# Performance work log

Hardware: AMD Instinct MI355X
Metric: run time of the kernel (lower is better)

Reference implementation:

```python
import jax
import jax.numpy as jnp
from jax import lax
import numpy as np

B, T, IN, H, K = 8, 4096, 512, 512, 2


def setup_inputs() -> dict:
    key = jax.random.key(0)
    k = jax.random.split(key, 5)
    scale_w0 = 1.0 / np.sqrt(IN * K)
    scale_w1 = 1.0 / np.sqrt(H * K)
    return {
        "x": jax.random.normal(k[0], (B, T, IN), jnp.float32),
        "w0": jax.random.normal(k[1], (3 * H, IN, K), jnp.float32) * scale_w0,
        "b0": jax.random.normal(k[2], (3 * H,), jnp.float32) * scale_w0,
        "w1": jax.random.normal(k[3], (3 * H, H, K), jnp.float32) * scale_w1,
        "b1": jax.random.normal(k[4], (3 * H,), jnp.float32) * scale_w1,
    }


def _qrnn_layer(x, w, b):
    # x: [B, T, C]; w: [3H, C, K]; causal conv (left pad K-1), matching
    # torch padding=K-1 then slicing off the last K-1 timesteps.
    xc = jnp.transpose(x, (0, 2, 1))  # [B, C, T]
    conv = lax.conv_general_dilated(
        xc, w, window_strides=(1,), padding=[(K - 1, 0)],
        dimension_numbers=("NCH", "OIH", "NCH"))
    conv = conv + b[None, :, None]
    conv = jnp.transpose(conv, (0, 2, 1))  # [B, T, 3H]
    z, f, o = jnp.split(conv, 3, axis=-1)
    z = jnp.tanh(z)
    f = jax.nn.sigmoid(f)
    o = jax.nn.sigmoid(o)

    def step(h, zfo):
        zt, ft, ot = zfo
        h = ft * h + (1.0 - ft) * zt  # fo-pool recurrence
        return h, ot * h

    h0 = jnp.zeros((x.shape[0], z.shape[-1]), x.dtype)
    hT, outs = lax.scan(
        step, h0,
        (jnp.swapaxes(z, 0, 1), jnp.swapaxes(f, 0, 1), jnp.swapaxes(o, 0, 1)))
    return jnp.swapaxes(outs, 0, 1), hT  # [B, T, H], [B, H]


def reference(x, w0, b0, w1, b1):
    out, h0 = _qrnn_layer(x, w0, b0)
    out, h1 = _qrnn_layer(out, w1, b1)
    return out, h0, h1
```

## Files before the change

### kernel.cpp

```cpp
#include <hip/hip_runtime.h>
#include <cstdint>

#define B_ 8
#define T_ 4096
#define TP1 4097
#define IN_ 512
#define H_ 512
#define N3H 1536
#define KD 1024
#define CHUNKS 64
#define CLEN 64
#define NT 16

typedef __attribute__((ext_vector_type(4))) float floatx4;
typedef __attribute__((ext_vector_type(4))) float f4;
typedef __attribute__((ext_vector_type(8))) short short8;
typedef __attribute__((ext_vector_type(4))) unsigned short us4;
typedef __attribute__((ext_vector_type(4))) _Float16 h4;

__device__ __forceinline__ unsigned short f2bf(float v){
  unsigned int u = __float_as_uint(v);
  unsigned int r = (u + 0x7fffu + ((u >> 16) & 1u)) >> 16;
  return (unsigned short)r;
}
__device__ __forceinline__ float sigm(float x){
  return __builtin_amdgcn_rcpf(1.f + __expf(-x));
}
__device__ __forceinline__ float tanhf_(float x){ return 2.f*sigm(2.f*x) - 1.f; }

#define GLLS(src, dst) __builtin_amdgcn_global_load_lds( \
    (const __attribute__((address_space(1))) void*)(src), \
    (__attribute__((address_space(3))) void*)(dst), 16, 0, 0)

__global__ void cast_pad_kernel(const float* __restrict__ x, unsigned short* __restrict__ xpad){
  int64_t i = (int64_t)blockIdx.x*256 + threadIdx.x;
  const int64_t total = (int64_t)B_*TP1*(IN_/4);
  if (i >= total) return;
  int cg = (int)(i & 127);
  int64_t r = i >> 7;
  int t = (int)(r % TP1);
  int b = (int)(r / TP1);
  us4 o;
  if (t == 0){ o = (us4){0,0,0,0}; }
  else {
    f4 v = *(const f4*)(x + ((int64_t)b*T_ + (t-1))*IN_ + cg*4);
    #pragma unroll
    for (int u=0;u<4;++u) o[u] = f2bf(v[u]);
  }
  *(us4*)(xpad + r*IN_ + cg*4) = o;
}

__global__ void wt_kernel(const float* __restrict__ wA, unsigned short* __restrict__ wtA,
                          const float* __restrict__ wB, unsigned short* __restrict__ wtB){
  int i = blockIdx.x*256 + threadIdx.x;
  if (i >= N3H*512) return;
  const float* w = blockIdx.y ? wB : wA;
  unsigned short* wt = blockIdx.y ? wtB : wtA;
  int ci = i & 511;
  int o = i >> 9;
  const float* wp = w + (int64_t)o*KD + ci*2;
  wt[(int64_t)o*KD + ci]       = f2bf(wp[0]);
  wt[(int64_t)o*KD + 512 + ci] = f2bf(wp[1]);
}

#define MFMA(a,b,c) __builtin_amdgcn_mfma_f32_16x16x32_bf16(a,b,c,0,0,0)
#define BAR() __builtin_amdgcn_s_barrier()

#define ST_A(tt, h) do { \
    const unsigned short* _s = aSrc + (h)*128*IN_ + (tt)*64; \
    unsigned short* _d = smem + ((tt)&1)*16384 + (h)*8192 + dstBase; \
    GLLS(_s, _d); GLLS(_s + 64*IN_, _d + 4096); } while(0)
#define ST_B(tt, h) do { \
    const unsigned short* _s = bSrc + (h)*128*KD + (tt)*64; \
    unsigned short* _d = smem + 32768 + ((tt)&1)*16384 + (h)*8192 + dstBase; \
    GLLS(_s, _d); GLLS(_s + 64*KD, _d + 4096); } while(0)

#define LDA(d,h,i,s) (*(const short8*)(smem + (d)*16384 + (h)*8192 + aRd + (i)*1024 + (s)))
#define LDB(d,h,i,s) (*(const short8*)(smem + (d)*16384 + (h)*8192 + bRd + (i)*1024 + (s)))

#define TILE(tc, SA1, SB1, SA0, SB0, VMN) do { \
  const int d_ = (tc) & 1; \
   \
  _Pragma("unroll") for (int i=0;i<4;++i){ aF[i][0]=LDA(d_,0,i,sw0); aF[i][1]=LDA(d_,0,i,sw1); } \
  _Pragma("unroll") for (int j=0;j<2;++j){ bF0[j][0]=LDB(d_,0,j,sw0); bF0[j][1]=LDB(d_,0,j,sw1); } \
  if (SA1) ST_A((tc)+1, 1); \
  BAR(); \
  __builtin_amdgcn_s_setprio(1); \
  _Pragma("unroll") for (int i=0;i<4;++i) _Pragma("unroll") for (int j=0;j<2;++j){ \
    acc[i][j]=MFMA(aF[i][0],bF0[j][0],acc[i][j]); acc[i][j]=MFMA(aF[i][1],bF0[j][1],acc[i][j]); } \
  __builtin_amdgcn_s_setprio(0); \
  BAR(); \
   \
  _Pragma("unroll") for (int j=0;j<2;++j){ bF1[j][0]=LDB(d_,1,j,sw0); bF1[j][1]=LDB(d_,1,j,sw1); } \
  if (SB1) ST_B((tc)+1, 1); \
  BAR(); \
  __builtin_amdgcn_s_setprio(1); \
  _Pragma("unroll") for (int i=0;i<4;++i) _Pragma("unroll") for (int j=0;j<2;++j){ \
    acc[i][2+j]=MFMA(aF[i][0],bF1[j][0],acc[i][2+j]); acc[i][2+j]=MFMA(aF[i][1],bF1[j][1],acc[i][2+j]); } \
  __builtin_amdgcn_s_setprio(0); \
  BAR(); \
   \
  _Pragma("unroll") for (int i=0;i<4;++i){ aF[i][0]=LDA(d_,1,i,sw0); aF[i][1]=LDA(d_,1,i,sw1); } \
  if (SA0) ST_A((tc)+2, 0); \
  BAR(); \
  __builtin_amdgcn_s_setprio(1); \
  _Pragma("unroll") for (int i=0;i<4;++i) _Pragma("unroll") for (int j=0;j<2;++j){ \
    acc[4+i][j]=MFMA(aF[i][0],bF0[j][0],acc[4+i][j]); acc[4+i][j]=MFMA(aF[i][1],bF0[j][1],acc[4+i][j]); } \
  __builtin_amdgcn_s_setprio(0); \
  BAR(); \
   \
  if (SB0) ST_B((tc)+2, 0); \
  BAR(); \
  __builtin_amdgcn_s_setprio(1); \
  _Pragma("unroll") for (int i=0;i<4;++i) _Pragma("unroll") for (int j=0;j<2;++j){ \
    acc[4+i][2+j]=MFMA(aF[i][0],bF1[j][0],acc[4+i][2+j]); acc[4+i][2+j]=MFMA(aF[i][1],bF1[j][1],acc[4+i][2+j]); } \
  __builtin_amdgcn_s_setprio(0); \
  if ((VMN)==4) asm volatile("s_waitcnt vmcnt(4)" ::: "memory"); \
  else if ((VMN)==0) asm volatile("s_waitcnt vmcnt(0)" ::: "memory"); \
  BAR(); \
} while(0)

__global__ __launch_bounds__(512, 2) void gemm_kernel(
    const unsigned short* __restrict__ A, const unsigned short* __restrict__ W,
    const float* __restrict__ bias, _Float16* __restrict__ C){
  __shared__ unsigned short smem[65536];
  const int tid  = threadIdx.x;
  const int lane = tid & 63;
  const int wave = tid >> 6;
  const int l16  = lane & 15;
  const int quad = lane >> 4;
  const int wm = wave >> 2;
  const int wn = wave & 3;
  const int lrow = lane >> 3;
  const int lcol = lane & 7;

  const int bid = blockIdx.x;
  const int wg = (bid & 7) * 96 + (bid >> 3);
  const int mt = wg / 6;
  const int nt = wg % 6;
  const int m0 = mt * 256;
  const int n0 = nt * 256;
  const int bb = m0 / T_;
  const int act = n0 >> 9;

  const unsigned short* aSrc = A + (int64_t)(m0 + bb + wave*8 + lrow)*IN_ + (lcol ^ lrow)*8;
  const unsigned short* bSrc = W + (int64_t)(n0 + wave*8 + lrow)*KD + (lcol ^ lrow)*8;
  const int dstBase = (wave*8 + lrow)*64 + lcol*8;

  const int sw0 = ( quad      ^ (l16 & 7)) * 8;
  const int sw1 = ((4 ^ quad) ^ (l16 & 7)) * 8;
  const int aRd = (wm*64 + l16)*64;
  const int bRd = 32768 + (wn*32 + l16)*64;

  floatx4 acc[8][4];
  #pragma unroll
  for (int i=0;i<8;i++)
    #pragma unroll
    for (int j=0;j<4;j++) acc[i][j] = (floatx4){0.f,0.f,0.f,0.f};
  short8 aF[4][2], bF0[2][2], bF1[2][2];

  ST_A(0,0); ST_B(0,0); ST_A(0,1); ST_B(0,1); ST_A(1,0); ST_B(1,0);
  asm volatile("s_waitcnt vmcnt(4)" ::: "memory");
  BAR();

  #pragma unroll 2
  for (int t = 0; t < NT-2; ++t){
    TILE(t, 1, 1, 1, 1, 4);
  }
  TILE(NT-2, 1, 1, 0, 0, 0);
  TILE(NT-1, 0, 0, 0, 0, -1);

  float bv[4];
  #pragma unroll
  for (int n=0;n<4;++n){
    const int cb = ((n&2)?128:0) + wn*32 + (n&1)*16;
    bv[n] = bias[n0 + cb + l16];
  }
  #pragma unroll
  for (int m=0;m<8;++m){
    const int rb = ((m&4)?128:0) + wm*64 + (m&3)*16;
    const int row = m0 + rb + quad*4;
    #pragma unroll
    for (int n=0;n<4;++n){
      const int cb = ((n&2)?128:0) + wn*32 + (n&1)*16;
      const int col = n0 + cb + l16;
      _Float16* cp = C + (int64_t)row*N3H + col;
      #pragma unroll
      for (int r=0;r<4;++r){
        float v = acc[m][n][r] + bv[n];
        v = (act == 0) ? tanhf_(v) : sigm(v);
        cp[(int64_t)r*N3H] = (_Float16)v;
      }
    }
  }
}

__global__ void scan_phase1(const _Float16* __restrict__ conv,
                            float* __restrict__ carA, float* __restrict__ carB){
  int q = blockIdx.x*256 + threadIdx.x;
  int chg = q & 127;
  int bq = (q >> 7) & 7;
  int c  = q >> 10;
  int ch = chg*4;
  f4 Aa = {1.f,1.f,1.f,1.f}, Bb = {0.f,0.f,0.f,0.f};
  const _Float16* p = conv + ((int64_t)bq*T_ + c*CLEN)*N3H + ch;
  for (int g=0; g<CLEN/8; ++g){
    h4 zb[8], fb[8];
    #pragma unroll
    for (int u=0;u<8;++u){
      zb[u] = *(const h4*)(p + (int64_t)u*N3H);
      fb[u] = *(const h4*)(p + (int64_t)u*N3H + 512);
    }
    #pragma unroll
    for (int u=0;u<8;++u){
      #pragma unroll
      for (int v=0;v<4;++v){
        float fv = (float)fb[u][v];
        float zv = (float)zb[u][v];
        Aa[v] *= fv;
        Bb[v] = fv*Bb[v] + (1.f-fv)*zv;
      }
    }
    p += (int64_t)8*N3H;
  }
  *(f4*)(carA + (int64_t)q*4) = Aa;
  *(f4*)(carB + (int64_t)q*4) = Bb;
}

__global__ void scan_phase2(const float* __restrict__ carA, const float* __restrict__ carB,
                            float* __restrict__ hstart, float* __restrict__ hT){
  int q = blockIdx.x*256 + threadIdx.x;
  float h = 0.f;
  for (int c=0;c<CHUNKS;++c){
    int64_t idx = (int64_t)c*4096 + q;
    hstart[idx] = h;
    h = carA[idx]*h + carB[idx];
  }
  hT[q] = h;
}

template<int LAYER>
__global__ void scan_phase3(const _Float16* __restrict__ conv,
                            const float* __restrict__ hstart, unsigned short* __restrict__ xpad,
                            float* __restrict__ outf){
  int q = blockIdx.x*256 + threadIdx.x;
  int chg = q & 127;
  int bq = (q >> 7) & 7;
  int c  = q >> 10;
  int ch = chg*4;
  f4 h;
  #pragma unroll
  for (int v=0;v<4;++v) h[v] = hstart[(int64_t)c*4096 + bq*512 + ch + v];
  const _Float16* p = conv + ((int64_t)bq*T_ + c*CLEN)*N3H + ch;
  int t = c*CLEN;
  for (int g=0; g<CLEN/8; ++g){
    h4 zb[8], fb[8], ob[8];
    #pragma unroll
    for (int u=0;u<8;++u){
      zb[u] = *(const h4*)(p + (int64_t)u*N3H);
      fb[u] = *(const h4*)(p + (int64_t)u*N3H + 512);
      ob[u] = *(const h4*)(p + (int64_t)u*N3H + 1024);
    }
    #pragma unroll
    for (int u=0;u<8;++u){
      if (LAYER == 0){
        us4 ov4;
        #pragma unroll
        for (int v=0;v<4;++v){
          float fv = (float)fb[u][v];
          h[v] = fv*h[v] + (1.f-fv)*(float)zb[u][v];
          ov4[v] = f2bf((float)ob[u][v]*h[v]);
        }
        *(us4*)(xpad + ((int64_t)bq*TP1 + t+u + 1)*IN_ + ch) = ov4;
      } else {
        f4 of4;
        #pragma unroll
        for (int v=0;v<4;++v){
          float fv = (float)fb[u][v];
          h[v] = fv*h[v] + (1.f-fv)*(float)zb[u][v];
          of4[v] = (float)ob[u][v]*h[v];
        }
        *(f4*)(outf + ((int64_t)bq*T_ + t+u)*H_ + ch) = of4;
      }
    }
    t += 8; p += (int64_t)8*N3H;
  }
}

extern "C" void kernel_launch(void* const* d_in, const int* in_sizes, int n_in,
                              void* d_out, int out_size, void* d_ws, size_t ws_size,
                              hipStream_t stream){
  const float* x  = (const float*)d_in[0];
  const float* w0 = (const float*)d_in[1];
  const float* b0 = (const float*)d_in[2];
  const float* w1 = (const float*)d_in[3];
  const float* b1 = (const float*)d_in[4];
  float* out = (float*)d_out;

  char* ws = (char*)d_ws;
  size_t off = 0;
  auto alloc = [&](size_t bytes)->char*{
    char* p = ws + off; off = (off + bytes + 255) & ~(size_t)255; return p; };
  unsigned short* xpad = (unsigned short*)alloc((size_t)B_*TP1*IN_*2);
  unsigned short* Wt0  = (unsigned short*)alloc((size_t)N3H*KD*2);
  unsigned short* Wt1  = (unsigned short*)alloc((size_t)N3H*KD*2);
  _Float16* conv = (_Float16*)alloc((size_t)B_*T_*N3H*2);
  float* carA = (float*)alloc((size_t)CHUNKS*4096*4);
  float* carB = (float*)alloc((size_t)CHUNKS*4096*4);
  float* hst  = (float*)alloc((size_t)CHUNKS*4096*4);
  if (off > ws_size) return;

  float* out_main = out;
  float* h0 = out + (int64_t)B_*T_*H_;
  float* h1 = h0 + B_*H_;

  const int64_t padN = (int64_t)B_*TP1*(IN_/4);
  cast_pad_kernel<<<(int)((padN + 255)/256), 256, 0, stream>>>(x, xpad);
  dim3 wgrid((N3H*512 + 255)/256, 2);
  wt_kernel<<<wgrid, 256, 0, stream>>>(w0, Wt0, w1, Wt1);

  const int ggrid = ((B_*T_)/256) * (N3H/256);
  const int sgrid = (CHUNKS*8*128) / 256;
  gemm_kernel<<<ggrid, 512, 0, stream>>>(xpad, Wt0, b0, conv);
  scan_phase1<<<sgrid, 256, 0, stream>>>(conv, carA, carB);
  scan_phase2<<<16, 256, 0, stream>>>(carA, carB, hst, h0);
  scan_phase3<0><<<sgrid, 256, 0, stream>>>(conv, hst, xpad, nullptr);

  gemm_kernel<<<ggrid, 512, 0, stream>>>(xpad, Wt1, b1, conv);
  scan_phase1<<<sgrid, 256, 0, stream>>>(conv, carA, carB);
  scan_phase2<<<16, 256, 0, stream>>>(carA, carB, hst, h1);
  scan_phase3<1><<<sgrid, 256, 0, stream>>>(conv, hst, nullptr, out_main);
}
```

Baseline: 414.6 us.

## Make GEMM persistent over three N tiles, prefetching next tile across boundaries

The GEMM grid is reduced from 768 blocks to 256, and each block loops over three consecutive 256-column N tiles for one M tile. The first two K-steps of the next N tile are prefetched during the tail of the current one, so the pipeline does not drain and refill between tiles. This is meant to cut the per-block prologue and epilogue cost and the tail idle time. In exchange, the epilogue stores and activations are serialized inside the block, and only 256 blocks are available to fill the CUs.

```diff
diff --git a/kernel.cpp b/kernel.cpp
--- a/kernel.cpp
+++ b/kernel.cpp
@@ -67,23 +67,24 @@
 #define BAR() __builtin_amdgcn_s_barrier()
 
 #define ST_A(tt, h) do { \
-    const unsigned short* _s = aSrc + (h)*128*IN_ + (tt)*64; \
+    const unsigned short* _s = aSrc + (h)*128*IN_ + ((tt)&(NT-1))*64; \
     unsigned short* _d = smem + ((tt)&1)*16384 + (h)*8192 + dstBase; \
     GLLS(_s, _d); GLLS(_s + 64*IN_, _d + 4096); } while(0)
-#define ST_B(tt, h) do { \
-    const unsigned short* _s = bSrc + (h)*128*KD + (tt)*64; \
+#define ST_BX(PTR, tt, h) do { \
+    const unsigned short* _s = (PTR) + (h)*128*KD + ((tt)&(NT-1))*64; \
     unsigned short* _d = smem + 32768 + ((tt)&1)*16384 + (h)*8192 + dstBase; \
     GLLS(_s, _d); GLLS(_s + 64*KD, _d + 4096); } while(0)
+#define ST_B(tt, h) ST_BX(bSrcC, tt, h)
 
 #define LDA(d,h,i,s) (*(const short8*)(smem + (d)*16384 + (h)*8192 + aRd + (i)*1024 + (s)))
 #define LDB(d,h,i,s) (*(const short8*)(smem + (d)*16384 + (h)*8192 + bRd + (i)*1024 + (s)))
 
-#define TILE(tc, SA1, SB1, SA0, SB0, VMN) do { \
+#define TILE(tc, S0, S1, S2, S3, VMN) do { \
   const int d_ = (tc) & 1; \
    \
   _Pragma("unroll") for (int i=0;i<4;++i){ aF[i][0]=LDA(d_,0,i,sw0); aF[i][1]=LDA(d_,0,i,sw1); } \
   _Pragma("unroll") for (int j=0;j<2;++j){ bF0[j][0]=LDB(d_,0,j,sw0); bF0[j][1]=LDB(d_,0,j,sw1); } \
-  if (SA1) ST_A((tc)+1, 1); \
+  S0; \
   BAR(); \
   __builtin_amdgcn_s_setprio(1); \
   _Pragma("unroll") for (int i=0;i<4;++i) _Pragma("unroll") for (int j=0;j<2;++j){ \
@@ -92,7 +93,7 @@
   BAR(); \
    \
   _Pragma("unroll") for (int j=0;j<2;++j){ bF1[j][0]=LDB(d_,1,j,sw0); bF1[j][1]=LDB(d_,1,j,sw1); } \
-  if (SB1) ST_B((tc)+1, 1); \
+  S1; \
   BAR(); \
   __builtin_amdgcn_s_setprio(1); \
   _Pragma("unroll") for (int i=0;i<4;++i) _Pragma("unroll") for (int j=0;j<2;++j){ \
@@ -101,7 +102,7 @@
   BAR(); \
    \
   _Pragma("unroll") for (int i=0;i<4;++i){ aF[i][0]=LDA(d_,1,i,sw0); aF[i][1]=LDA(d_,1,i,sw1); } \
-  if (SA0) ST_A((tc)+2, 0); \
+  S2; \
   BAR(); \
   __builtin_amdgcn_s_setprio(1); \
   _Pragma("unroll") for (int i=0;i<4;++i) _Pragma("unroll") for (int j=0;j<2;++j){ \
@@ -109,7 +110,7 @@
   __builtin_amdgcn_s_setprio(0); \
   BAR(); \
    \
-  if (SB0) ST_B((tc)+2, 0); \
+  S3; \
   BAR(); \
   __builtin_amdgcn_s_setprio(1); \
   _Pragma("unroll") for (int i=0;i<4;++i) _Pragma("unroll") for (int j=0;j<2;++j){ \
@@ -135,16 +136,14 @@
   const int lcol = lane & 7;
 
   const int bid = blockIdx.x;
-  const int wg = (bid & 7) * 96 + (bid >> 3);
-  const int mt = wg / 6;
-  const int nt = wg % 6;
+  const int p = (bid & 7) * 32 + (bid >> 3);
+  const int mt = p >> 1;
+  const int mhalf = p & 1;
   const int m0 = mt * 256;
-  const int n0 = nt * 256;
   const int bb = m0 / T_;
-  const int act = n0 >> 9;
 
   const unsigned short* aSrc = A + (int64_t)(m0 + bb + wave*8 + lrow)*IN_ + (lcol ^ lrow)*8;
-  const unsigned short* bSrc = W + (int64_t)(n0 + wave*8 + lrow)*KD + (lcol ^ lrow)*8;
+  const unsigned short* bSrcC = W + (int64_t)(mhalf*3*256 + wave*8 + lrow)*KD + (lcol ^ lrow)*8;
   const int dstBase = (wave*8 + lrow)*64 + lcol*8;
 
   const int sw0 = ( quad      ^ (l16 & 7)) * 8;
@@ -153,45 +152,58 @@
   const int bRd = 32768 + (wn*32 + l16)*64;
 
   floatx4 acc[8][4];
-  #pragma unroll
-  for (int i=0;i<8;i++)
-    #pragma unroll
-    for (int j=0;j<4;j++) acc[i][j] = (floatx4){0.f,0.f,0.f,0.f};
   short8 aF[4][2], bF0[2][2], bF1[2][2];
 
   ST_A(0,0); ST_B(0,0); ST_A(0,1); ST_B(0,1); ST_A(1,0); ST_B(1,0);
   asm volatile("s_waitcnt vmcnt(4)" ::: "memory");
   BAR();
 
-  #pragma unroll 2
-  for (int t = 0; t < NT-2; ++t){
-    TILE(t, 1, 1, 1, 1, 4);
-  }
-  TILE(NT-2, 1, 1, 0, 0, 0);
-  TILE(NT-1, 0, 0, 0, 0, -1);
-
-  float bv[4];
-  #pragma unroll
-  for (int n=0;n<4;++n){
-    const int cb = ((n&2)?128:0) + wn*32 + (n&1)*16;
-    bv[n] = bias[n0 + cb + l16];
-  }
-  #pragma unroll
-  for (int m=0;m<8;++m){
-    const int rb = ((m&4)?128:0) + wm*64 + (m&3)*16;
-    const int row = m0 + rb + quad*4;
+  for (int mi = 0; mi < 3; ++mi){
+    #pragma unroll
+    for (int i=0;i<8;i++)
+      #pragma unroll
+      for (int j=0;j<4;j++) acc[i][j] = (floatx4){0.f,0.f,0.f,0.f};
+
+    const unsigned short* bSrcN = bSrcC + (int64_t)256*KD;
+
+    #pragma unroll 2
+    for (int t = 0; t < NT-2; ++t)
+      TILE(t, ST_A(t+1,1), ST_B(t+1,1), ST_A(t+2,0), ST_B(t+2,0), 4);
+
+    if (mi < 2){
+      TILE(NT-2, ST_A(NT-1,1), ST_B(NT-1,1), ST_A(NT,0),   ST_BX(bSrcN,NT,0),   4);
+      TILE(NT-1, ST_A(NT,1),   ST_BX(bSrcN,NT,1), ST_A(NT+1,0), ST_BX(bSrcN,NT+1,0), 4);
+    } else {
+      TILE(NT-2, ST_A(NT-1,1), ST_B(NT-1,1), (void)0, (void)0, 0);
+      TILE(NT-1, (void)0, (void)0, (void)0, (void)0, -1);
+    }
+
+    const int n0 = (mhalf*3 + mi) * 256;
+    const int act = n0 >> 9;
+    float bv[4];
     #pragma unroll
     for (int n=0;n<4;++n){
       const int cb = ((n&2)?128:0) + wn*32 + (n&1)*16;
-      const int col = n0 + cb + l16;
-      _Float16* cp = C + (int64_t)row*N3H + col;
+      bv[n] = bias[n0 + cb + l16];
+    }
+    #pragma unroll
+    for (int m=0;m<8;++m){
+      const int rb = ((m&4)?128:0) + wm*64 + (m&3)*16;
+      const int row = m0 + rb + quad*4;
       #pragma unroll
-      for (int r=0;r<4;++r){
-        float v = acc[m][n][r] + bv[n];
-        v = (act == 0) ? tanhf_(v) : sigm(v);
-        cp[(int64_t)r*N3H] = (_Float16)v;
+      for (int n=0;n<4;++n){
+        const int cb = ((n&2)?128:0) + wn*32 + (n&1)*16;
+        const int col = n0 + cb + l16;
+        _Float16* cp = C + (int64_t)row*N3H + col;
+        #pragma unroll
+        for (int r=0;r<4;++r){
+          float v = acc[m][n][r] + bv[n];
+          v = (act == 0) ? tanhf_(v) : sigm(v);
+          cp[(int64_t)r*N3H] = (_Float16)v;
+        }
       }
     }
+    bSrcC = bSrcN;
   }
 }
 
@@ -319,7 +331,7 @@
   dim3 wgrid((N3H*512 + 255)/256, 2);
   wt_kernel<<<wgrid, 256, 0, stream>>>(w0, Wt0, w1, Wt1);
 
-  const int ggrid = ((B_*T_)/256) * (N3H/256);
+  const int ggrid = 256;
   const int sgrid = (CHUNKS*8*128) / 256;
   gemm_kernel<<<ggrid, 512, 0, stream>>>(xpad, Wt0, b0, conv);
   scan_phase1<<<sgrid, 256, 0, stream>>>(conv, carA, carB);
```

Result: slower. 565.9 us (+36.5%).

## Fuse scan phases into one kernel with grid barriers and merge prep kernels

Applied to the files above, without the earlier changes.

Merges the three scan phases into a single persistent kernel of 256 blocks that synchronises through atomic grid barriers instead of separate kernel launches. The cast/pad and weight-transpose kernels are also merged into one prep kernel, which zeroes the barrier counters. This removes launch gaps and kernel boundaries between small scan kernels. It relies on all 256 blocks being co-resident and adds spin-wait overhead, with a deadlock risk if they are not.

```diff
diff --git a/kernel.cpp b/kernel.cpp
--- a/kernel.cpp
+++ b/kernel.cpp
@@ -11,6 +11,7 @@
 #define CHUNKS 64
 #define CLEN 64
 #define NT 16
+#define NBLK 256
 
 typedef __attribute__((ext_vector_type(4))) float floatx4;
 typedef __attribute__((ext_vector_type(4))) float f4;
@@ -32,35 +33,38 @@
     (const __attribute__((address_space(1))) void*)(src), \
     (__attribute__((address_space(3))) void*)(dst), 16, 0, 0)
 
-__global__ void cast_pad_kernel(const float* __restrict__ x, unsigned short* __restrict__ xpad){
+__global__ void prep_kernel(const float* __restrict__ x, unsigned short* __restrict__ xpad,
+                            const float* __restrict__ w0, unsigned short* __restrict__ Wt0,
+                            const float* __restrict__ w1, unsigned short* __restrict__ Wt1,
+                            int* __restrict__ bar){
+  if (blockIdx.x == 0 && threadIdx.x < 4) bar[threadIdx.x] = 0;
   int64_t i = (int64_t)blockIdx.x*256 + threadIdx.x;
-  const int64_t total = (int64_t)B_*TP1*(IN_/4);
-  if (i >= total) return;
-  int cg = (int)(i & 127);
-  int64_t r = i >> 7;
-  int t = (int)(r % TP1);
-  int b = (int)(r / TP1);
-  us4 o;
-  if (t == 0){ o = (us4){0,0,0,0}; }
-  else {
-    f4 v = *(const f4*)(x + ((int64_t)b*T_ + (t-1))*IN_ + cg*4);
-    #pragma unroll
-    for (int u=0;u<4;++u) o[u] = f2bf(v[u]);
-  }
-  *(us4*)(xpad + r*IN_ + cg*4) = o;
-}
-
-__global__ void wt_kernel(const float* __restrict__ wA, unsigned short* __restrict__ wtA,
-                          const float* __restrict__ wB, unsigned short* __restrict__ wtB){
-  int i = blockIdx.x*256 + threadIdx.x;
-  if (i >= N3H*512) return;
-  const float* w = blockIdx.y ? wB : wA;
-  unsigned short* wt = blockIdx.y ? wtB : wtA;
-  int ci = i & 511;
-  int o = i >> 9;
-  const float* wp = w + (int64_t)o*KD + ci*2;
-  wt[(int64_t)o*KD + ci]       = f2bf(wp[0]);
-  wt[(int64_t)o*KD + 512 + ci] = f2bf(wp[1]);
+  const int64_t castN = (int64_t)B_*TP1*(IN_/4);
+  if (i < castN){
+    int cg = (int)(i & 127);
+    int64_t r = i >> 7;
+    int t = (int)(r % TP1);
+    int b = (int)(r / TP1);
+    us4 o;
+    if (t == 0){ o = (us4){0,0,0,0}; }
+    else {
+      f4 v = *(const f4*)(x + ((int64_t)b*T_ + (t-1))*IN_ + cg*4);
+      #pragma unroll
+      for (int u=0;u<4;++u) o[u] = f2bf(v[u]);
+    }
+    *(us4*)(xpad + r*IN_ + cg*4) = o;
+  } else {
+    int64_t j = i - castN;
+    int layer = (j >= (int64_t)N3H*512);
+    int jj = (int)(j - (int64_t)layer*N3H*512);
+    const float* w = layer ? w1 : w0;
+    unsigned short* wt = layer ? Wt1 : Wt0;
+    int ci = jj & 511;
+    int o = jj >> 9;
+    const float* wp = w + (int64_t)o*KD + ci*2;
+    wt[(int64_t)o*KD + ci]       = f2bf(wp[0]);
+    wt[(int64_t)o*KD + 512 + ci] = f2bf(wp[1]);
+  }
 }
 
 #define MFMA(a,b,c) __builtin_amdgcn_mfma_f32_16x16x32_bf16(a,b,c,0,0,0)
@@ -195,95 +199,106 @@
   }
 }
 
-__global__ void scan_phase1(const _Float16* __restrict__ conv,
-                            float* __restrict__ carA, float* __restrict__ carB){
-  int q = blockIdx.x*256 + threadIdx.x;
-  int chg = q & 127;
-  int bq = (q >> 7) & 7;
-  int c  = q >> 10;
-  int ch = chg*4;
-  f4 Aa = {1.f,1.f,1.f,1.f}, Bb = {0.f,0.f,0.f,0.f};
-  const _Float16* p = conv + ((int64_t)bq*T_ + c*CLEN)*N3H + ch;
-  for (int g=0; g<CLEN/8; ++g){
-    h4 zb[8], fb[8];
-    #pragma unroll
-    for (int u=0;u<8;++u){
-      zb[u] = *(const h4*)(p + (int64_t)u*N3H);
-      fb[u] = *(const h4*)(p + (int64_t)u*N3H + 512);
-    }
-    #pragma unroll
-    for (int u=0;u<8;++u){
-      #pragma unroll
-      for (int v=0;v<4;++v){
-        float fv = (float)fb[u][v];
-        float zv = (float)zb[u][v];
-        Aa[v] *= fv;
-        Bb[v] = fv*Bb[v] + (1.f-fv)*zv;
-      }
-    }
-    p += (int64_t)8*N3H;
-  }
-  *(f4*)(carA + (int64_t)q*4) = Aa;
-  *(f4*)(carB + (int64_t)q*4) = Bb;
-}
-
-__global__ void scan_phase2(const float* __restrict__ carA, const float* __restrict__ carB,
-                            float* __restrict__ hstart, float* __restrict__ hT){
-  int q = blockIdx.x*256 + threadIdx.x;
-  float h = 0.f;
-  for (int c=0;c<CHUNKS;++c){
-    int64_t idx = (int64_t)c*4096 + q;
-    hstart[idx] = h;
-    h = carA[idx]*h + carB[idx];
-  }
-  hT[q] = h;
+__device__ __forceinline__ void gridbar(int* bar, int id){
+  __syncthreads();
+  if (threadIdx.x == 0){
+    __threadfence();
+    atomicAdd(&bar[id], 1);
+    while (atomicAdd(&bar[id], 0) < NBLK) __builtin_amdgcn_s_sleep(8);
+    __threadfence();
+  }
+  __syncthreads();
 }
 
 template<int LAYER>
-__global__ void scan_phase3(const _Float16* __restrict__ conv,
-                            const float* __restrict__ hstart, unsigned short* __restrict__ xpad,
-                            float* __restrict__ outf){
-  int q = blockIdx.x*256 + threadIdx.x;
-  int chg = q & 127;
-  int bq = (q >> 7) & 7;
-  int c  = q >> 10;
-  int ch = chg*4;
-  f4 h;
-  #pragma unroll
-  for (int v=0;v<4;++v) h[v] = hstart[(int64_t)c*4096 + bq*512 + ch + v];
-  const _Float16* p = conv + ((int64_t)bq*T_ + c*CLEN)*N3H + ch;
-  int t = c*CLEN;
-  for (int g=0; g<CLEN/8; ++g){
-    h4 zb[8], fb[8], ob[8];
-    #pragma unroll
-    for (int u=0;u<8;++u){
-      zb[u] = *(const h4*)(p + (int64_t)u*N3H);
-      fb[u] = *(const h4*)(p + (int64_t)u*N3H + 512);
-      ob[u] = *(const h4*)(p + (int64_t)u*N3H + 1024);
-    }
-    #pragma unroll
-    for (int u=0;u<8;++u){
-      if (LAYER == 0){
-        us4 ov4;
+__global__ void scan_fused(const _Float16* __restrict__ conv,
+                           float* __restrict__ carA, float* __restrict__ carB,
+                           float* __restrict__ hstart, float* __restrict__ hT,
+                           unsigned short* __restrict__ xpad, float* __restrict__ outf,
+                           int* __restrict__ bar){
+  const int q = blockIdx.x*256 + threadIdx.x;
+  const int chg = q & 127;
+  const int bq = (q >> 7) & 7;
+  const int c  = q >> 10;
+  const int ch = chg*4;
+  const _Float16* pbase = conv + ((int64_t)bq*T_ + c*CLEN)*N3H + ch;
+
+  {
+    f4 Aa = {1.f,1.f,1.f,1.f}, Bb = {0.f,0.f,0.f,0.f};
+    const _Float16* p = pbase;
+    for (int g=0; g<CLEN/8; ++g){
+      h4 zb[8], fb[8];
+      #pragma unroll
+      for (int u=0;u<8;++u){
+        zb[u] = *(const h4*)(p + (int64_t)u*N3H);
+        fb[u] = *(const h4*)(p + (int64_t)u*N3H + 512);
+      }
+      #pragma unroll
+      for (int u=0;u<8;++u){
         #pragma unroll
         for (int v=0;v<4;++v){
           float fv = (float)fb[u][v];
-          h[v] = fv*h[v] + (1.f-fv)*(float)zb[u][v];
-          ov4[v] = f2bf((float)ob[u][v]*h[v]);
+          float zv = (float)zb[u][v];
+          Aa[v] *= fv;
+          Bb[v] = fv*Bb[v] + (1.f-fv)*zv;
         }
-        *(us4*)(xpad + ((int64_t)bq*TP1 + t+u + 1)*IN_ + ch) = ov4;
-      } else {
-        f4 of4;
-        #pragma unroll
-        for (int v=0;v<4;++v){
-          float fv = (float)fb[u][v];
-          h[v] = fv*h[v] + (1.f-fv)*(float)zb[u][v];
-          of4[v] = (float)ob[u][v]*h[v];
+      }
+      p += (int64_t)8*N3H;
+    }
+    *(f4*)(carA + (int64_t)q*4) = Aa;
+    *(f4*)(carB + (int64_t)q*4) = Bb;
+  }
+  gridbar(bar, 2*LAYER);
+
+  if (blockIdx.x < 16){
+    float h = 0.f;
+    for (int cc=0;cc<CHUNKS;++cc){
+      int64_t idx = (int64_t)cc*4096 + q;
+      hstart[idx] = h;
+      h = carA[idx]*h + carB[idx];
+    }
+    hT[q] = h;
+  }
+  gridbar(bar, 2*LAYER+1);
+
+  {
+    f4 h;
+    #pragma unroll
+    for (int v=0;v<4;++v) h[v] = hstart[(int64_t)c*4096 + bq*512 + ch + v];
+    const _Float16* p = pbase;
+    int t = c*CLEN;
+    for (int g=0; g<CLEN/8; ++g){
+      h4 zb[8], fb[8], ob[8];
+      #pragma unroll
+      for (int u=0;u<8;++u){
+        zb[u] = *(const h4*)(p + (int64_t)u*N3H);
+        fb[u] = *(const h4*)(p + (int64_t)u*N3H + 512);
+        ob[u] = *(const h4*)(p + (int64_t)u*N3H + 1024);
+      }
+      #pragma unroll
+      for (int u=0;u<8;++u){
+        if (LAYER == 0){
+          us4 ov4;
+          #pragma unroll
+          for (int v=0;v<4;++v){
+            float fv = (float)fb[u][v];
+            h[v] = fv*h[v] + (1.f-fv)*(float)zb[u][v];
+            ov4[v] = f2bf((float)ob[u][v]*h[v]);
+          }
+          *(us4*)(xpad + ((int64_t)bq*TP1 + t+u + 1)*IN_ + ch) = ov4;
+        } else {
+          f4 of4;
+          #pragma unroll
+          for (int v=0;v<4;++v){
+            float fv = (float)fb[u][v];
+            h[v] = fv*h[v] + (1.f-fv)*(float)zb[u][v];
+            of4[v] = (float)ob[u][v]*h[v];
+          }
+          *(f4*)(outf + ((int64_t)bq*T_ + t+u)*H_ + ch) = of4;
         }
-        *(f4*)(outf + ((int64_t)bq*T_ + t+u)*H_ + ch) = of4;
-      }
-    }
-    t += 8; p += (int64_t)8*N3H;
+      }
+      t += 8; p += (int64_t)8*N3H;
+    }
   }
 }
 
@@ -308,26 +323,21 @@
   float* carA = (float*)alloc((size_t)CHUNKS*4096*4);
   float* carB = (float*)alloc((size_t)CHUNKS*4096*4);
   float* hst  = (float*)alloc((size_t)CHUNKS*4096*4);
+  int*   bar  = (int*)alloc(4*sizeof(int));
   if (off > ws_size) return;
 
   float* out_main = out;
   float* h0 = out + (int64_t)B_*T_*H_;
   float* h1 = h0 + B_*H_;
 
-  const int64_t padN = (int64_t)B_*TP1*(IN_/4);
-  cast_pad_kernel<<<(int)((padN + 255)/256), 256, 0, stream>>>(x, xpad);
-  dim3 wgrid((N3H*512 + 255)/256, 2);
-  wt_kernel<<<wgrid, 256, 0, stream>>>(w0, Wt0, w1, Wt1);
+  const int64_t castN = (int64_t)B_*TP1*(IN_/4);
+  const int64_t prepN = castN + (int64_t)2*N3H*512;
+  prep_kernel<<<(int)((prepN + 255)/256), 256, 0, stream>>>(x, xpad, w0, Wt0, w1, Wt1, bar);
 
   const int ggrid = ((B_*T_)/256) * (N3H/256);
-  const int sgrid = (CHUNKS*8*128) / 256;
   gemm_kernel<<<ggrid, 512, 0, stream>>>(xpad, Wt0, b0, conv);
-  scan_phase1<<<sgrid, 256, 0, stream>>>(conv, carA, carB);
-  scan_phase2<<<16, 256, 0, stream>>>(carA, carB, hst, h0);
-  scan_phase3<0><<<sgrid, 256, 0, stream>>>(conv, hst, xpad, nullptr);
+  scan_fused<0><<<NBLK, 256, 0, stream>>>(conv, carA, carB, hst, h0, xpad, nullptr, bar);
 
   gemm_kernel<<<ggrid, 512, 0, stream>>>(xpad, Wt1, b1, conv);
-  scan_phase1<<<sgrid, 256, 0, stream>>>(conv, carA, carB);
-  scan_phase2<<<16, 256, 0, stream>>>(carA, carB, hst, h1);
-  scan_phase3<1><<<sgrid, 256, 0, stream>>>(conv, hst, nullptr, out_main);
-}
+  scan_fused<1><<<NBLK, 256, 0, stream>>>(conv, carA, carB, hst, h1, nullptr, out_main, bar);
+}
```

Measured after the change: 461.9 us. 11.4% more time.
